# Kernel tuning notes

Measured on AMD Instinct MI355X. Metric: run time of the kernel, lower is better.

## Reference

```python
import jax, jax.numpy as jnp
import numpy as np

B, S, D, H = 2, 2048, 2048, 16
HD = D // H  # head_dim = 128


def setup_inputs() -> dict:
    key = jax.random.key(0)
    ks = jax.random.split(key, 9)
    std = 0.02
    x = jax.random.normal(ks[0], (B, S, D), dtype=jnp.float32)
    Wq = jax.random.normal(ks[1], (D, D), dtype=jnp.float32) * std
    bq = jnp.zeros((D,), dtype=jnp.float32)
    Wk = jax.random.normal(ks[2], (D, D), dtype=jnp.float32) * std
    bk = jnp.zeros((D,), dtype=jnp.float32)
    Wv = jax.random.normal(ks[3], (D, D), dtype=jnp.float32) * std
    bv = jnp.zeros((D,), dtype=jnp.float32)
    Wo = jax.random.normal(ks[4], (D, D), dtype=jnp.float32) * std
    bo = jnp.zeros((D,), dtype=jnp.float32)
    return {"x": x, "Wq": Wq, "bq": bq, "Wk": Wk, "bk": bk,
            "Wv": Wv, "bv": bv, "Wo": Wo, "bo": bo}


def _rope_tables(seq_len, head_dim, base=10000.0):
    # inv_freq over even indices; freqs: [S, HD/2]
    inv_freq = 1.0 / (base ** (jnp.arange(0, head_dim, 2, dtype=jnp.float32) / head_dim))
    t = jnp.arange(seq_len, dtype=jnp.float32)
    freqs = jnp.einsum('i,j->ij', t, inv_freq)
    return jnp.cos(freqs), jnp.sin(freqs)  # each [S, HD/2]


def _rotate(x, cos, sin):
    # x: [B, H, S, HD]; cos/sin: [S, HD/2] broadcast over B,H
    x1, x2 = jnp.split(x, 2, axis=-1)
    return jnp.concatenate([x1 * cos - x2 * sin, x1 * sin + x2 * cos], axis=-1)


def reference(x, Wq, bq, Wk, bk, Wv, bv, Wo, bo):
    b, s, d = x.shape
    q = (jnp.einsum('bsd,df->bsf', x, Wq) + bq).reshape(b, s, H, HD).transpose(0, 2, 1, 3)
    k = (jnp.einsum('bsd,df->bsf', x, Wk) + bk).reshape(b, s, H, HD).transpose(0, 2, 1, 3)
    v = (jnp.einsum('bsd,df->bsf', x, Wv) + bv).reshape(b, s, H, HD).transpose(0, 2, 1, 3)
    cos, sin = _rope_tables(s, HD)
    qr = _rotate(q, cos, sin)
    kr = _rotate(k, cos, sin)
    scores = jnp.einsum('bhqd,bhkd->bhqk', qr, kr) / jnp.sqrt(jnp.float32(HD))
    probs = jax.nn.softmax(scores, axis=-1)
    out = jnp.einsum('bhqk,bhkd->bhqd', probs, v)
    out = out.transpose(0, 2, 1, 3).reshape(b, s, d)
    return jnp.einsum('bsd,df->bsf', out, Wo) + bo
```

## Files before the change

### kernel.cpp

```cpp
#include <hip/hip_runtime.h>

#define BB  2
#define SS  2048
#define DD  2048
#define HH  16
#define HDD 128
#define BSR 4096

using short8  = __attribute__((ext_vector_type(8))) short;
using floatx4 = __attribute__((ext_vector_type(4))) float;

__device__ __forceinline__ float bf2f(unsigned short u) {
  return __uint_as_float(((unsigned int)u) << 16);
}
__device__ __forceinline__ unsigned short f2bf(float f) {
  unsigned int u = __float_as_uint(f);
  u += 0x7fffu + ((u >> 16) & 1u);
  return (unsigned short)(u >> 16);
}
__device__ __forceinline__ unsigned int pk2bf(float a, float b) {
  unsigned int ua = __float_as_uint(a);
  ua += 0x7fffu + ((ua >> 16) & 1u);
  unsigned int ub = __float_as_uint(b);
  ub += 0x7fffu + ((ub >> 16) & 1u);
  return (ua >> 16) | (ub & 0xffff0000u);
}
__device__ __forceinline__ float fexp2(float x) {
#if __has_builtin(__builtin_amdgcn_exp2f)
  return __builtin_amdgcn_exp2f(x);
#else
  return __expf(x * 0.6931471805599453f);
#endif
}
__device__ __forceinline__ void gl_lds16(const void* g, void* l) {
  __builtin_amdgcn_global_load_lds(
      (__attribute__((address_space(1))) void*)g,
      (__attribute__((address_space(3))) void*)l, 16, 0, 0);
}

__global__ __launch_bounds__(256) void transpose_w(
    const float* __restrict__ Wq, const float* __restrict__ Wk,
    const float* __restrict__ Wv, const float* __restrict__ Wo,
    unsigned short* __restrict__ wqkvt, unsigned short* __restrict__ wot)
{
  __shared__ float tile[32][33];
  const float* W; unsigned short* Out;
  int z = blockIdx.z;
  if      (z == 0) { W = Wq; Out = wqkvt; }
  else if (z == 1) { W = Wk; Out = wqkvt + (size_t)DD * DD; }
  else if (z == 2) { W = Wv; Out = wqkvt + 2 * (size_t)DD * DD; }
  else             { W = Wo; Out = wot; }
  int tx = threadIdx.x, ty = threadIdx.y;
  int d0 = blockIdx.y * 32, f0 = blockIdx.x * 32;
#pragma unroll
  for (int i = 0; i < 4; i++)
    tile[ty + i * 8][tx] = W[(size_t)(d0 + ty + i * 8) * DD + f0 + tx];
  __syncthreads();
#pragma unroll
  for (int i = 0; i < 4; i++)
    Out[(size_t)(f0 + ty + i * 8) * DD + d0 + tx] = f2bf(tile[tx][ty + i * 8]);
}

__global__ __launch_bounds__(256) void conv_x(const float* __restrict__ x,
                                              unsigned short* __restrict__ xb)
{
  size_t i = ((size_t)blockIdx.x * 256 + threadIdx.x) * 4;
  float4 v = *(const float4*)(x + i);
  ushort4 o;
  o.x = f2bf(v.x); o.y = f2bf(v.y); o.z = f2bf(v.z); o.w = f2bf(v.w);
  *(ushort4*)(xb + i) = o;
}

__global__ __launch_bounds__(256) void rope_tab(float2* __restrict__ rtab) {
  int idx = blockIdx.x * 256 + threadIdx.x;
  int s = idx >> 6, c = idx & 63;
  float inv = powf(10000.f, -(float)c * (1.f / 64.f));
  float ang = (float)s * inv;
  float sn, cc;
  sincosf(ang, &sn, &cc);
  rtab[idx] = make_float2(cc, sn);
}

__global__ __launch_bounds__(256) void gemm_qkv(
    const unsigned short* __restrict__ A, const unsigned short* __restrict__ Bt,
    const float* __restrict__ bq, const float* __restrict__ bk,
    const float* __restrict__ bv, const float2* __restrict__ rtab,
    unsigned short* __restrict__ q_r, unsigned short* __restrict__ k_r,
    unsigned short* __restrict__ v_t)
{
  __shared__ unsigned short smem[16896];
  unsigned short* As = smem;
  unsigned short* Bs = smem + 8192;
  const int K = DD;
  int t = threadIdx.x;
  int m0 = blockIdx.y * 128, n0 = blockIdx.x * 128;
  int w = t >> 6, lane = t & 63, qd = lane >> 4, l16 = lane & 15;
  int wm = (w >> 1) * 64, wn = (w & 1) * 64;
  floatx4 zero4 = {0.f, 0.f, 0.f, 0.f};
  floatx4 acc[4][4];
#pragma unroll
  for (int i = 0; i < 4; i++)
#pragma unroll
    for (int j = 0; j < 4; j++) acc[i][j] = zero4;

  int gchunk = (t & 7) ^ ((t >> 3) & 7);
  const unsigned short* Ab = A  + (size_t)(m0 + (t >> 3)) * K + gchunk * 8;
  const unsigned short* Bb = Bt + (size_t)(n0 + (t >> 3)) * K + gchunk * 8;
  size_t qK = (size_t)32 * K;

  for (int k0 = 0; k0 < K; k0 += 64) {
    __syncthreads();
#pragma unroll
    for (int c = 0; c < 4; c++) {
      gl_lds16(Ab + c * qK + k0, &As[(c * 256 + t) * 8]);
      gl_lds16(Bb + c * qK + k0, &Bs[(c * 256 + t) * 8]);
    }
    __syncthreads();
#pragma unroll
    for (int ks = 0; ks < 2; ks++) {
      int ch = ((ks * 4 + qd) ^ (l16 & 7)) * 8;
      short8 af[4], bfr[4];
#pragma unroll
      for (int i = 0; i < 4; i++)
        af[i] = *(const short8*)&As[(wm + i * 16 + l16) * 64 + ch];
#pragma unroll
      for (int j = 0; j < 4; j++)
        bfr[j] = *(const short8*)&Bs[(wn + j * 16 + l16) * 64 + ch];
#pragma unroll
      for (int i = 0; i < 4; i++)
#pragma unroll
        for (int j = 0; j < 4; j++)
          acc[i][j] = __builtin_amdgcn_mfma_f32_16x16x32_bf16(af[i], bfr[j], acc[i][j], 0, 0, 0);
    }
  }

  int plane = n0 >> 11;
  int h = (n0 >> 7) & 15;
  const float* bias = plane == 0 ? bq : (plane == 1 ? bk : bv);
  __syncthreads();
#pragma unroll
  for (int i = 0; i < 4; i++)
#pragma unroll
    for (int j = 0; j < 4; j++) {
      int rl = wm + i * 16 + qd * 4;
      int cl = wn + j * 16 + l16;
      float bsv = bias[h * 128 + cl];
#pragma unroll
      for (int r = 0; r < 4; r++)
        smem[(rl + r) * 132 + cl] = f2bf(acc[i][j][r] + bsv);
    }
  __syncthreads();

  int b = m0 >> 11, sbase = m0 & (SS - 1);
  if (plane < 2) {
    unsigned short* dst = (plane == 0 ? q_r : k_r) + (size_t)(b * HH + h) * SS * HDD;
    const float fac = (plane == 0) ? 0.12751744f : 1.0f;
#pragma unroll
    for (int it = 0; it < 16; it++) {
      int idx = it * 256 + t;
      int rl = idx >> 5, c2 = (idx & 31) * 2;
      int s = sbase + rl;
      float4 cs = *(const float4*)&rtab[(size_t)s * 64 + c2];
      float a0 = bf2f(smem[rl * 132 + c2]);
      float a1 = bf2f(smem[rl * 132 + c2 + 1]);
      float b0 = bf2f(smem[rl * 132 + c2 + 64]);
      float b1 = bf2f(smem[rl * 132 + c2 + 65]);
      unsigned int lo = pk2bf((a0 * cs.x - b0 * cs.y) * fac,
                              (a1 * cs.z - b1 * cs.w) * fac);
      unsigned int hi = pk2bf((a0 * cs.y + b0 * cs.x) * fac,
                              (a1 * cs.w + b1 * cs.z) * fac);
      size_t rowb = (size_t)s * HDD;
      *(unsigned int*)&dst[rowb + c2]      = lo;
      *(unsigned int*)&dst[rowb + c2 + 64] = hi;
    }
  } else {
    unsigned short* dst = v_t + (size_t)(b * HH + h) * HDD * SS;
#pragma unroll
    for (int it = 0; it < 32; it++) {
      int idx = it * 256 + t;
      int hd = idx >> 6, sp = (idx & 63) * 2;
      unsigned short v0 = smem[sp * 132 + hd];
      unsigned short v1 = smem[(sp + 1) * 132 + hd];
      int y = sp & 63;
      int kap = ((y >> 5) & 1) * 32 + ((y >> 2) & 3) * 8 + ((y >> 4) & 1) * 4 + (y & 3);
      int sg = sbase + (sp & ~63) + kap;
      *(unsigned int*)&dst[(size_t)hd * SS + sg] = ((unsigned int)v1 << 16) | v0;
    }
  }
}

template <bool OUTF32>
__global__ __launch_bounds__(256) void gemm_bt(
    const unsigned short* __restrict__ A, const unsigned short* __restrict__ Bt,
    const float* __restrict__ bias, void* __restrict__ Cout,
    int M, int N, int K)
{
  __shared__ unsigned short As[128 * 64];
  __shared__ unsigned short Bs[128 * 64];
  int t = threadIdx.x;
  int m0 = blockIdx.y * 128, n0 = blockIdx.x * 128;
  int w = t >> 6, lane = t & 63, qd = lane >> 4, l16 = lane & 15;
  int wm = (w >> 1) * 64, wn = (w & 1) * 64;
  floatx4 zero4 = {0.f, 0.f, 0.f, 0.f};
  floatx4 acc[4][4];
#pragma unroll
  for (int i = 0; i < 4; i++)
#pragma unroll
    for (int j = 0; j < 4; j++) acc[i][j] = zero4;

  int gchunk = (t & 7) ^ ((t >> 3) & 7);
  const unsigned short* Ab = A  + (size_t)(m0 + (t >> 3)) * K + gchunk * 8;
  const unsigned short* Bb = Bt + (size_t)(n0 + (t >> 3)) * K + gchunk * 8;
  size_t qK = (size_t)32 * K;

  for (int k0 = 0; k0 < K; k0 += 64) {
    __syncthreads();
#pragma unroll
    for (int c = 0; c < 4; c++) {
      gl_lds16(Ab + c * qK + k0, &As[(c * 256 + t) * 8]);
      gl_lds16(Bb + c * qK + k0, &Bs[(c * 256 + t) * 8]);
    }
    __syncthreads();
#pragma unroll
    for (int ks = 0; ks < 2; ks++) {
      int ch = ((ks * 4 + qd) ^ (l16 & 7)) * 8;
      short8 af[4], bfr[4];
#pragma unroll
      for (int i = 0; i < 4; i++)
        af[i] = *(const short8*)&As[(wm + i * 16 + l16) * 64 + ch];
#pragma unroll
      for (int j = 0; j < 4; j++)
        bfr[j] = *(const short8*)&Bs[(wn + j * 16 + l16) * 64 + ch];
#pragma unroll
      for (int i = 0; i < 4; i++)
#pragma unroll
        for (int j = 0; j < 4; j++)
          acc[i][j] = __builtin_amdgcn_mfma_f32_16x16x32_bf16(af[i], bfr[j], acc[i][j], 0, 0, 0);
    }
  }

#pragma unroll
  for (int i = 0; i < 4; i++)
#pragma unroll
    for (int j = 0; j < 4; j++) {
      int row = m0 + wm + i * 16 + qd * 4;
      int col = n0 + wn + j * 16 + l16;
      float bsv = bias ? bias[col] : 0.f;
#pragma unroll
      for (int r = 0; r < 4; r++) {
        float v = acc[i][j][r] + bsv;
        if (OUTF32) ((float*)Cout)[(size_t)(row + r) * N + col] = v;
        else ((unsigned short*)Cout)[(size_t)(row + r) * N + col] = f2bf(v);
      }
    }
}

__global__ __launch_bounds__(256, 2) void attn_kernel(
    const unsigned short* __restrict__ q_r, const unsigned short* __restrict__ k_r,
    const unsigned short* __restrict__ v_t, unsigned short* __restrict__ aout)
{
  __shared__ unsigned short Ks[2][64 * 128];
  __shared__ unsigned short Vs[2][128 * 64];
  int t = threadIdx.x, w = t >> 6, lane = t & 63, qd = lane >> 4, l16 = lane & 15;
  int L = blockIdx.y * gridDim.x + blockIdx.x;
  int jj = L >> 3;
  int bh = (L & 7) * 4 + (jj >> 4);
  int q0 = (jj & 15) * 128;
  const unsigned short* qb = q_r + (size_t)bh * SS * HDD;
  const unsigned short* kb = k_r + (size_t)bh * SS * HDD;
  const unsigned short* vb = v_t + (size_t)bh * HDD * SS;

  short8 aq[2][4];
#pragma unroll
  for (int mi = 0; mi < 2; mi++)
#pragma unroll
    for (int ks = 0; ks < 4; ks++)
      aq[mi][ks] = *(const short8*)
          &qb[(size_t)(q0 + w * 32 + mi * 16 + l16) * HDD + ks * 32 + qd * 8];

  float m_i[2], l_i[2];
  floatx4 zero4 = {0.f, 0.f, 0.f, 0.f};
  floatx4 o[2][8];
#pragma unroll
  for (int mi = 0; mi < 2; mi++) { m_i[mi] = -1e30f; l_i[mi] = 0.f; }
#pragma unroll
  for (int mi = 0; mi < 2; mi++)
#pragma unroll
    for (int n = 0; n < 8; n++) o[mi][n] = zero4;

  auto stage = [&](int nb, int kt) {
#pragma unroll
    for (int c = 0; c < 4; c++) {
      int flat = c * 256 + t;
      int r = flat >> 4, cc = flat & 15;
      gl_lds16(kb + (size_t)(kt + r) * HDD + (cc ^ (r & 15)) * 8, &Ks[nb][flat * 8]);
    }
#pragma unroll
    for (int c = 0; c < 4; c++) {
      int flat = c * 256 + t;
      int r = flat >> 3, cc = flat & 7;
      gl_lds16(vb + (size_t)r * SS + kt + (cc ^ (r & 7)) * 8, &Vs[nb][flat * 8]);
    }
  };

  stage(0, 0);
  int buf = 0;

  for (int kt = 0; kt < SS; kt += 64) {
    __syncthreads();
    if (kt + 64 < SS) stage(buf ^ 1, kt + 64);

    floatx4 sc[2][4];
#pragma unroll
    for (int mi = 0; mi < 2; mi++)
#pragma unroll
      for (int j = 0; j < 4; j++) sc[mi][j] = zero4;
#pragma unroll
    for (int j = 0; j < 4; j++) {
      int krow = j * 16 + l16;
#pragma unroll
      for (int ks = 0; ks < 4; ks++) {
        int chunk = ks * 4 + qd;
        short8 kf = *(const short8*)&Ks[buf][krow * 128 + ((chunk ^ (krow & 15)) * 8)];
        sc[0][j] = __builtin_amdgcn_mfma_f32_16x16x32_bf16(kf, aq[0][ks], sc[0][j], 0, 0, 0);
        sc[1][j] = __builtin_amdgcn_mfma_f32_16x16x32_bf16(kf, aq[1][ks], sc[1][j], 0, 0, 0);
      }
    }

    float rmax[2];
#pragma unroll
    for (int mi = 0; mi < 2; mi++) {
      float m = sc[mi][0][0];
#pragma unroll
      for (int j = 0; j < 4; j++)
#pragma unroll
        for (int r = 0; r < 4; r++) m = fmaxf(m, sc[mi][j][r]);
      m = fmaxf(m, __shfl_xor(m, 16, 64));
      m = fmaxf(m, __shfl_xor(m, 32, 64));
      rmax[mi] = m;
    }

    bool up = (rmax[0] > m_i[0]) || (rmax[1] > m_i[1]);
    if (__ballot(up) != 0ull) {
#pragma unroll
      for (int mi = 0; mi < 2; mi++) {
        float mn = fmaxf(m_i[mi], rmax[mi]);
        float a = fexp2(m_i[mi] - mn);
        m_i[mi] = mn;
        l_i[mi] *= a;
#pragma unroll
        for (int n = 0; n < 8; n++)
#pragma unroll
          for (int r = 0; r < 4; r++) o[mi][n][r] *= a;
      }
    }

    unsigned int pr[2][4][2];
#pragma unroll
    for (int mi = 0; mi < 2; mi++) {
      float s0 = 0.f;
#pragma unroll
      for (int j = 0; j < 4; j++) {
        float p0 = fexp2(sc[mi][j][0] - m_i[mi]);
        float p1 = fexp2(sc[mi][j][1] - m_i[mi]);
        float p2 = fexp2(sc[mi][j][2] - m_i[mi]);
        float p3 = fexp2(sc[mi][j][3] - m_i[mi]);
        s0 += (p0 + p1) + (p2 + p3);
        pr[mi][j][0] = pk2bf(p0, p1);
        pr[mi][j][1] = pk2bf(p2, p3);
      }
      s0 += __shfl_xor(s0, 16, 64);
      s0 += __shfl_xor(s0, 32, 64);
      l_i[mi] += s0;
    }

#pragma unroll
    for (int n = 0; n < 8; n++) {
      int vrow = n * 16 + l16;
#pragma unroll
      for (int ks = 0; ks < 2; ks++) {
        int chunk = ks * 4 + qd;
        short8 av = *(const short8*)&Vs[buf][vrow * 64 + ((chunk ^ (vrow & 7)) * 8)];
        union { unsigned int u[4]; short8 v; } bp0, bp1;
        bp0.u[0] = pr[0][2 * ks][0];     bp0.u[1] = pr[0][2 * ks][1];
        bp0.u[2] = pr[0][2 * ks + 1][0]; bp0.u[3] = pr[0][2 * ks + 1][1];
        bp1.u[0] = pr[1][2 * ks][0];     bp1.u[1] = pr[1][2 * ks][1];
        bp1.u[2] = pr[1][2 * ks + 1][0]; bp1.u[3] = pr[1][2 * ks + 1][1];
        o[0][n] = __builtin_amdgcn_mfma_f32_16x16x32_bf16(av, bp0.v, o[0][n], 0, 0, 0);
        o[1][n] = __builtin_amdgcn_mfma_f32_16x16x32_bf16(av, bp1.v, o[1][n], 0, 0, 0);
      }
    }
    buf ^= 1;
  }

  int b = bh >> 4, h = bh & 15;
#pragma unroll
  for (int mi = 0; mi < 2; mi++) {
    int qrow = q0 + w * 32 + mi * 16 + l16;
    float inv_l = 1.f / l_i[mi];
    size_t base = ((size_t)(b * SS + qrow)) * DD + h * HDD;
#pragma unroll
    for (int n = 0; n < 8; n++) {
      uint2 pkd;
      pkd.x = pk2bf(o[mi][n][0] * inv_l, o[mi][n][1] * inv_l);
      pkd.y = pk2bf(o[mi][n][2] * inv_l, o[mi][n][3] * inv_l);
      *(uint2*)&aout[base + n * 16 + qd * 4] = pkd;
    }
  }
}

extern "C" void kernel_launch(void* const* d_in, const int* in_sizes, int n_in,
                              void* d_out, int out_size, void* d_ws, size_t ws_size,
                              hipStream_t stream) {
  const float* x  = (const float*)d_in[0];
  const float* Wq = (const float*)d_in[1];
  const float* bq = (const float*)d_in[2];
  const float* Wk = (const float*)d_in[3];
  const float* bk = (const float*)d_in[4];
  const float* Wv = (const float*)d_in[5];
  const float* bv = (const float*)d_in[6];
  const float* Wo = (const float*)d_in[7];
  const float* bo = (const float*)d_in[8];
  float* out = (float*)d_out;

  char* ws = (char*)d_ws;
  unsigned short* xb      = (unsigned short*)(ws + 0);
  unsigned short* wqkvt   = (unsigned short*)(ws + 16777216);
  unsigned short* wot     = (unsigned short*)(ws + 41943040);
  float2*         rtab    = (float2*)(ws + 50331648);
  unsigned short* q_r     = (unsigned short*)(ws + 100663296);
  unsigned short* k_r     = (unsigned short*)(ws + 117440512);
  unsigned short* v_t     = (unsigned short*)(ws + 134217728);
  unsigned short* attn_o  = xb;

  transpose_w<<<dim3(DD / 32, DD / 32, 4), dim3(32, 8), 0, stream>>>(
      Wq, Wk, Wv, Wo, wqkvt, wot);
  conv_x<<<dim3((BSR * DD) / 1024), dim3(256), 0, stream>>>(x, xb);
  rope_tab<<<dim3((SS * 64) / 256), dim3(256), 0, stream>>>(rtab);
  gemm_qkv<<<dim3(3 * DD / 128, BSR / 128), dim3(256), 0, stream>>>(
      xb, wqkvt, bq, bk, bv, rtab, q_r, k_r, v_t);
  attn_kernel<<<dim3(SS / 128, BB * HH), dim3(256), 0, stream>>>(
      q_r, k_r, v_t, attn_o);
  gemm_bt<true><<<dim3(DD / 128, BSR / 128), dim3(256), 0, stream>>>(
      attn_o, wot, bo, out, BSR, DD, DD);
}
```

Before: 398.7 us.

## Rewrite QKV GEMM with 256x256 tiles, 8 waves, and double-buffered ping-pong pipeline

The QKV projection GEMM moves from 128x128 tiles with 4 waves to 256x256 tiles with 8 waves and 128 KB of LDS, split into two double-buffered A/B stages. Global-to-LDS loads are interleaved with MFMA quads under explicit barriers, vmcnt waits and s_setprio, so load latency overlaps compute. Block IDs are remapped for cache locality, and the epilogue now writes the bias+RoPE or V-transpose output in two halves to fit LDS. This raises data reuse per tile and reduces barrier stalls, but it limits occupancy to one block per CU and the grid shrinks to 384 blocks.

After: 411.7 us. 1.03x slower.

```diff
diff --git a/kernel.cpp b/kernel.cpp
--- a/kernel.cpp
+++ b/kernel.cpp
@@ -81,111 +81,218 @@
   rtab[idx] = make_float2(cc, sn);
 }
 
-__global__ __launch_bounds__(256) void gemm_qkv(
+#define MFMA_QUAD(MB, NB, FB) \
+  _Pragma("unroll") for (int m_ = 0; m_ < 4; m_++) \
+  _Pragma("unroll") for (int n_ = 0; n_ < 2; n_++) \
+  _Pragma("unroll") for (int kk_ = 0; kk_ < 2; kk_++) \
+    acc[(MB)+m_][(NB)+n_] = __builtin_amdgcn_mfma_f32_16x16x32_bf16( \
+        fa[m_][kk_], FB[n_][kk_], acc[(MB)+m_][(NB)+n_], 0, 0, 0);
+#define BARX __builtin_amdgcn_s_barrier()
+
+__global__ __launch_bounds__(512) void gemm_qkv(
     const unsigned short* __restrict__ A, const unsigned short* __restrict__ Bt,
     const float* __restrict__ bq, const float* __restrict__ bk,
     const float* __restrict__ bv, const float2* __restrict__ rtab,
     unsigned short* __restrict__ q_r, unsigned short* __restrict__ k_r,
     unsigned short* __restrict__ v_t)
 {
-  __shared__ unsigned short smem[16896];
-  unsigned short* As = smem;
-  unsigned short* Bs = smem + 8192;
+  __shared__ unsigned short smem[65536];
+  unsigned short* const AsP[2] = { smem,         smem + 32768 };
+  unsigned short* const BsP[2] = { smem + 16384, smem + 49152 };
   const int K = DD;
   int t = threadIdx.x;
-  int m0 = blockIdx.y * 128, n0 = blockIdx.x * 128;
-  int w = t >> 6, lane = t & 63, qd = lane >> 4, l16 = lane & 15;
-  int wm = (w >> 1) * 64, wn = (w & 1) * 64;
+  int lane = t & 63, qd = lane >> 4, l16 = lane & 15;
+  int w = t >> 6, wr = w >> 2, wc = w & 3;
+
+  int bid = blockIdx.y * gridDim.x + blockIdx.x;
+  int wg  = (bid & 7) * 48 + (bid >> 3);
+  int n0 = (wg % 24) * 256;
+  int m0 = (wg / 24) * 256;
+
   floatx4 zero4 = {0.f, 0.f, 0.f, 0.f};
-  floatx4 acc[4][4];
-#pragma unroll
-  for (int i = 0; i < 4; i++)
+  floatx4 acc[8][4];
+#pragma unroll
+  for (int i = 0; i < 8; i++)
 #pragma unroll
     for (int j = 0; j < 4; j++) acc[i][j] = zero4;
 
-  int gchunk = (t & 7) ^ ((t >> 3) & 7);
-  const unsigned short* Ab = A  + (size_t)(m0 + (t >> 3)) * K + gchunk * 8;
-  const unsigned short* Bb = Bt + (size_t)(n0 + (t >> 3)) * K + gchunk * 8;
-  size_t qK = (size_t)32 * K;
-
-  for (int k0 = 0; k0 < K; k0 += 64) {
+  int srow = t >> 3;
+  int schunk = ((t & 7) ^ (srow & 7)) * 8;
+  const unsigned short* Ag = A  + (size_t)(m0 + srow) * K + schunk;
+  const unsigned short* Bg = Bt + (size_t)(n0 + srow) * K + schunk;
+
+  auto stA = [&](int bf, int kt, int half) {
+#pragma unroll
+    for (int q = 0; q < 2; q++) {
+      int c = half * 2 + q;
+      gl_lds16(Ag + (size_t)c * 64 * K + kt * 64, AsP[bf] + ((size_t)c * 512 + t) * 8);
+    }
+  };
+  auto stB = [&](int bf, int kt, int half) {
+#pragma unroll
+    for (int q = 0; q < 2; q++) {
+      int c = half * 2 + q;
+      gl_lds16(Bg + (size_t)c * 64 * K + kt * 64, BsP[bf] + ((size_t)c * 512 + t) * 8);
+    }
+  };
+  auto ldA = [&](int bf, int mf, int kk) -> short8 {
+    int row = wr * 128 + mf * 16 + l16;
+    return *(const short8*)&AsP[bf][row * 64 + (((kk * 4 + qd) ^ (l16 & 7)) * 8)];
+  };
+  auto ldB = [&](int bf, int nf, int kk) -> short8 {
+    int row = wc * 64 + nf * 16 + l16;
+    return *(const short8*)&BsP[bf][row * 64 + (((kk * 4 + qd) ^ (l16 & 7)) * 8)];
+  };
+
+  stA(0, 0, 0); stA(0, 0, 1); stB(0, 0, 0); stB(0, 0, 1);
+  stA(1, 1, 0);
+  asm volatile("s_waitcnt vmcnt(2)" ::: "memory");
+  BARX;
+
+  short8 fa[4][2], fbl[2][2], fbh[2][2];
+
+#pragma unroll 1
+  for (int i = 0; i < 16; i++) {
+    const bool full = (i < 15);
+    const int kt1 = 2 * i + 1, kt2 = 2 * i + 2, kt3 = 2 * i + 3;
+
+#pragma unroll
+    for (int m = 0; m < 4; m++) { fa[m][0] = ldA(0, m, 0); fa[m][1] = ldA(0, m, 1); }
+#pragma unroll
+    for (int n = 0; n < 2; n++) { fbl[n][0] = ldB(0, n, 0); fbl[n][1] = ldB(0, n, 1); }
+    stA(1, kt1, 1);
+    BARX;
+    __builtin_amdgcn_s_setprio(1);
+    MFMA_QUAD(0, 0, fbl);
+    __builtin_amdgcn_s_setprio(0);
+    BARX;
+#pragma unroll
+    for (int n = 0; n < 2; n++) { fbh[n][0] = ldB(0, 2 + n, 0); fbh[n][1] = ldB(0, 2 + n, 1); }
+    stB(1, kt1, 0);
+    BARX;
+    __builtin_amdgcn_s_setprio(1);
+    MFMA_QUAD(0, 2, fbh);
+    __builtin_amdgcn_s_setprio(0);
+    BARX;
+#pragma unroll
+    for (int m = 0; m < 4; m++) { fa[m][0] = ldA(0, 4 + m, 0); fa[m][1] = ldA(0, 4 + m, 1); }
+    stB(1, kt1, 1);
+    BARX;
+    __builtin_amdgcn_s_setprio(1);
+    MFMA_QUAD(4, 0, fbl);
+    __builtin_amdgcn_s_setprio(0);
+    BARX;
+    if (full) stA(0, kt2, 0);
+    BARX;
+    __builtin_amdgcn_s_setprio(1);
+    MFMA_QUAD(4, 2, fbh);
+    __builtin_amdgcn_s_setprio(0);
+    if (full) asm volatile("s_waitcnt vmcnt(2)" ::: "memory");
+    else      asm volatile("s_waitcnt vmcnt(0)" ::: "memory");
+    BARX;
+
+#pragma unroll
+    for (int m = 0; m < 4; m++) { fa[m][0] = ldA(1, m, 0); fa[m][1] = ldA(1, m, 1); }
+#pragma unroll
+    for (int n = 0; n < 2; n++) { fbl[n][0] = ldB(1, n, 0); fbl[n][1] = ldB(1, n, 1); }
+    if (full) stA(0, kt2, 1);
+    BARX;
+    __builtin_amdgcn_s_setprio(1);
+    MFMA_QUAD(0, 0, fbl);
+    __builtin_amdgcn_s_setprio(0);
+    BARX;
+#pragma unroll
+    for (int n = 0; n < 2; n++) { fbh[n][0] = ldB(1, 2 + n, 0); fbh[n][1] = ldB(1, 2 + n, 1); }
+    if (full) stB(0, kt2, 0);
+    BARX;
+    __builtin_amdgcn_s_setprio(1);
+    MFMA_QUAD(0, 2, fbh);
+    __builtin_amdgcn_s_setprio(0);
+    BARX;
+#pragma unroll
+    for (int m = 0; m < 4; m++) { fa[m][0] = ldA(1, 4 + m, 0); fa[m][1] = ldA(1, 4 + m, 1); }
+    if (full) stB(0, kt2, 1);
+    BARX;
+    __builtin_amdgcn_s_setprio(1);
+    MFMA_QUAD(4, 0, fbl);
+    __builtin_amdgcn_s_setprio(0);
+    BARX;
+    if (full) stA(1, kt3, 0);
+    BARX;
+    __builtin_amdgcn_s_setprio(1);
+    MFMA_QUAD(4, 2, fbh);
+    __builtin_amdgcn_s_setprio(0);
+    if (full) asm volatile("s_waitcnt vmcnt(2)" ::: "memory");
+    else      asm volatile("s_waitcnt vmcnt(0)" ::: "memory");
+    BARX;
+  }
+
+  __syncthreads();
+  int plane = n0 >> 11;
+  int h0 = (n0 >> 7) & 15;
+  const float* bias = plane == 0 ? bq : (plane == 1 ? bk : bv);
+  int bI = m0 >> 11, sbase = m0 & (SS - 1);
+  const int CT = 258;
+  unsigned short* Ct = smem;
+
+#pragma unroll 1
+  for (int half = 0; half < 2; half++) {
+    if (wr == half) {
+#pragma unroll
+      for (int mf = 0; mf < 8; mf++)
+#pragma unroll
+        for (int nf = 0; nf < 4; nf++) {
+          int rl = mf * 16 + qd * 4;
+          int cl = wc * 64 + nf * 16 + l16;
+          float bsv = bias[h0 * 128 + cl];
+#pragma unroll
+          for (int r = 0; r < 4; r++)
+            Ct[(rl + r) * CT + cl] = f2bf(acc[mf][nf][r] + bsv);
+        }
+    }
     __syncthreads();
-#pragma unroll
-    for (int c = 0; c < 4; c++) {
-      gl_lds16(Ab + c * qK + k0, &As[(c * 256 + t) * 8]);
-      gl_lds16(Bb + c * qK + k0, &Bs[(c * 256 + t) * 8]);
-    }
-    __syncthreads();
-#pragma unroll
-    for (int ks = 0; ks < 2; ks++) {
-      int ch = ((ks * 4 + qd) ^ (l16 & 7)) * 8;
-      short8 af[4], bfr[4];
-#pragma unroll
-      for (int i = 0; i < 4; i++)
-        af[i] = *(const short8*)&As[(wm + i * 16 + l16) * 64 + ch];
-#pragma unroll
-      for (int j = 0; j < 4; j++)
-        bfr[j] = *(const short8*)&Bs[(wn + j * 16 + l16) * 64 + ch];
-#pragma unroll
-      for (int i = 0; i < 4; i++)
-#pragma unroll
-        for (int j = 0; j < 4; j++)
-          acc[i][j] = __builtin_amdgcn_mfma_f32_16x16x32_bf16(af[i], bfr[j], acc[i][j], 0, 0, 0);
-    }
-  }
-
-  int plane = n0 >> 11;
-  int h = (n0 >> 7) & 15;
-  const float* bias = plane == 0 ? bq : (plane == 1 ? bk : bv);
-  __syncthreads();
-#pragma unroll
-  for (int i = 0; i < 4; i++)
-#pragma unroll
-    for (int j = 0; j < 4; j++) {
-      int rl = wm + i * 16 + qd * 4;
-      int cl = wn + j * 16 + l16;
-      float bsv = bias[h * 128 + cl];
-#pragma unroll
-      for (int r = 0; r < 4; r++)
-        smem[(rl + r) * 132 + cl] = f2bf(acc[i][j][r] + bsv);
-    }
-  __syncthreads();
-
-  int b = m0 >> 11, sbase = m0 & (SS - 1);
-  if (plane < 2) {
-    unsigned short* dst = (plane == 0 ? q_r : k_r) + (size_t)(b * HH + h) * SS * HDD;
-    const float fac = (plane == 0) ? 0.12751744f : 1.0f;
-#pragma unroll
-    for (int it = 0; it < 16; it++) {
-      int idx = it * 256 + t;
-      int rl = idx >> 5, c2 = (idx & 31) * 2;
-      int s = sbase + rl;
-      float4 cs = *(const float4*)&rtab[(size_t)s * 64 + c2];
-      float a0 = bf2f(smem[rl * 132 + c2]);
-      float a1 = bf2f(smem[rl * 132 + c2 + 1]);
-      float b0 = bf2f(smem[rl * 132 + c2 + 64]);
-      float b1 = bf2f(smem[rl * 132 + c2 + 65]);
-      unsigned int lo = pk2bf((a0 * cs.x - b0 * cs.y) * fac,
-                              (a1 * cs.z - b1 * cs.w) * fac);
-      unsigned int hi = pk2bf((a0 * cs.y + b0 * cs.x) * fac,
-                              (a1 * cs.w + b1 * cs.z) * fac);
-      size_t rowb = (size_t)s * HDD;
-      *(unsigned int*)&dst[rowb + c2]      = lo;
-      *(unsigned int*)&dst[rowb + c2 + 64] = hi;
-    }
-  } else {
-    unsigned short* dst = v_t + (size_t)(b * HH + h) * HDD * SS;
-#pragma unroll
-    for (int it = 0; it < 32; it++) {
-      int idx = it * 256 + t;
-      int hd = idx >> 6, sp = (idx & 63) * 2;
-      unsigned short v0 = smem[sp * 132 + hd];
-      unsigned short v1 = smem[(sp + 1) * 132 + hd];
-      int y = sp & 63;
-      int kap = ((y >> 5) & 1) * 32 + ((y >> 2) & 3) * 8 + ((y >> 4) & 1) * 4 + (y & 3);
-      int sg = sbase + (sp & ~63) + kap;
-      *(unsigned int*)&dst[(size_t)hd * SS + sg] = ((unsigned int)v1 << 16) | v0;
-    }
+    if (plane < 2) {
+      unsigned short* dst0 = (plane == 0 ? q_r : k_r) + (size_t)(bI * HH + h0) * SS * HDD;
+      const float fac = (plane == 0) ? 0.12751744f : 1.0f;
+#pragma unroll
+      for (int it = 0; it < 16; it++) {
+        int idx = it * 512 + t;
+        int rl = idx >> 6;
+        int u = idx & 63; int hh = u >> 5; int c2 = (u & 31) * 2;
+        int s = sbase + half * 128 + rl;
+        float4 cs = *(const float4*)&rtab[(size_t)s * 64 + c2];
+        int cb = hh * 128 + c2;
+        float a0 = bf2f(Ct[rl * CT + cb]);
+        float a1 = bf2f(Ct[rl * CT + cb + 1]);
+        float b0 = bf2f(Ct[rl * CT + cb + 64]);
+        float b1 = bf2f(Ct[rl * CT + cb + 65]);
+        unsigned int lo = pk2bf((a0 * cs.x - b0 * cs.y) * fac,
+                                (a1 * cs.z - b1 * cs.w) * fac);
+        unsigned int hi = pk2bf((a0 * cs.y + b0 * cs.x) * fac,
+                                (a1 * cs.w + b1 * cs.z) * fac);
+        unsigned short* dst = dst0 + (size_t)hh * SS * HDD;
+        size_t rowb = (size_t)s * HDD;
+        *(unsigned int*)&dst[rowb + c2]      = lo;
+        *(unsigned int*)&dst[rowb + c2 + 64] = hi;
+      }
+    } else {
+      unsigned short* dst0 = v_t + (size_t)(bI * HH + h0) * HDD * SS;
+#pragma unroll
+      for (int it = 0; it < 32; it++) {
+        int idx = it * 512 + t;
+        int hdg = idx >> 6;
+        int sp = (idx & 63) * 2;
+        unsigned short v0 = Ct[sp * CT + hdg];
+        unsigned short v1 = Ct[(sp + 1) * CT + hdg];
+        int hh = hdg >> 7, hd = hdg & 127;
+        int y = sp & 63;
+        int kap = ((y >> 5) & 1) * 32 + ((y >> 2) & 3) * 8 + ((y >> 4) & 1) * 4 + (y & 3);
+        int sg = sbase + half * 128 + (sp & ~63) + kap;
+        unsigned short* dst = dst0 + (size_t)hh * HDD * SS;
+        *(unsigned int*)&dst[(size_t)hd * SS + sg] = ((unsigned int)v1 << 16) | v0;
+      }
+    }
+    if (half == 0) __syncthreads();
   }
 }
 
@@ -437,7 +544,7 @@
       Wq, Wk, Wv, Wo, wqkvt, wot);
   conv_x<<<dim3((BSR * DD) / 1024), dim3(256), 0, stream>>>(x, xb);
   rope_tab<<<dim3((SS * 64) / 256), dim3(256), 0, stream>>>(rtab);
-  gemm_qkv<<<dim3(3 * DD / 128, BSR / 128), dim3(256), 0, stream>>>(
+  gemm_qkv<<<dim3(3 * DD / 256, BSR / 256), dim3(512), 0, stream>>>(
       xb, wqkvt, bq, bk, bv, rtab, q_r, k_r, v_t);
   attn_kernel<<<dim3(SS / 128, BB * HH), dim3(256), 0, stream>>>(
       q_r, k_r, v_t, attn_o);
```
